# Optimization experiments

Measured on AMD Instinct MI355X. Metric: run time of the kernel, lower is better.

The kernel has to match this reference:

```python
import jax, jax.numpy as jnp
import numpy as np

D_MODEL = 1024
SEQ_LEN = 2048
NUM_EIGH = 24
BATCH = 4


def _spectral_filters(L, K):
    # Hankel matrix Z[i,j] = 2 / ((i+j)^3 - (i+j)), 1-indexed; top-K eigvecs scaled by sigma^0.25
    t = np.arange(1, L + 1, dtype=np.float64)
    s = t[:, None] + t[None, :]
    Z = 2.0 / (s ** 3 - s)
    sigma, phi = np.linalg.eigh(Z)
    phi_k = phi[:, -K:] * (sigma[-K:] ** 0.25)
    return jnp.asarray(phi_k, dtype=jnp.float32)


def setup_inputs() -> dict:
    key = jax.random.key(0)
    k1, k2, k3 = jax.random.split(key, 3)
    std = 1.0 / np.sqrt(D_MODEL)
    return {
        "x": jax.random.normal(k1, (BATCH, SEQ_LEN, D_MODEL), dtype=jnp.float32),
        "M_inputs": jax.random.normal(k2, (D_MODEL, D_MODEL), dtype=jnp.float32) * std,
        "M_filters": jax.random.normal(k3, (NUM_EIGH, D_MODEL), dtype=jnp.float32) * std,
        "phi": _spectral_filters(SEQ_LEN, NUM_EIGH),
    }


def _convolve_approx(u, v, n):
    # u: [B, L, D] inputs (already projected); v: [L, D] per-channel causal filters.
    # Dual-branch causal FFT convolution:
    #   plus[b,t,d]  = sum_{s<=t} v[s,d] * u[b,t-s,d]
    #   minus[b,t,d] = (-1)^t * sum_{s<=t} v[s,d] * (-1)^{t-s} u[b,t-s,d]
    B, L, D = u.shape
    sgn = jnp.where(jnp.arange(L) % 2 == 0, 1.0, -1.0).astype(u.dtype)[None, :, None]  # [1,L,1]
    V = jnp.fft.rfft(v, n=n, axis=0)                     # [F, D] complex
    U = jnp.stack([u, u * sgn], axis=-1)                 # [B, L, D, 2]
    Uf = jnp.fft.rfft(U, n=n, axis=1)                    # [B, F, D, 2]
    conv = jnp.fft.irfft(V[None, :, :, None] * Uf, n=n, axis=1)[:, :L]  # [B, L, D, 2]
    return conv[..., 0], conv[..., 1] * sgn


def reference(x, M_inputs, M_filters, phi):
    L = x.shape[1]
    n = 1 << int(np.ceil(np.log2(2 * L - 1)))  # next pow2 of 2L-1 (static)
    x_proj = x @ M_inputs                       # [B, L, D]
    phi_proj = phi[:L] @ M_filters              # [L, D]
    spectral_plus, spectral_minus = _convolve_approx(x_proj, phi_proj, n)
    return spectral_plus + spectral_minus
```

## Files before the change

kernel.cpp:

```cpp
#include <hip/hip_runtime.h>
#include <stdint.h>

#define D_MODEL 1024
#define SEQ 2048
#define HALF 1024
#define K_EIG 24
#define GUARD4 24
#define K4 128
#define K4P (GUARD4 + K4)
#define WE_JP4 72

typedef __attribute__((ext_vector_type(8))) short bf16x8;
typedef __attribute__((ext_vector_type(4))) float f32x4;
typedef _Float16 f16;
typedef _Float16 f16x2 __attribute__((ext_vector_type(2)));
typedef unsigned int uint;

#define GAS __attribute__((address_space(1)))
#define LAS __attribute__((address_space(3)))

static __device__ __forceinline__ unsigned short f2bf(float f) {
  union { float f; uint32_t u; } v; v.f = f;
  uint32_t u = v.u;
  u += 0x7FFFu + ((u >> 16) & 1u);
  return (unsigned short)(u >> 16);
}

static __device__ __forceinline__ float dot2(uint w2, uint u2, float c) {
  return __builtin_amdgcn_fdot2(__builtin_bit_cast(f16x2, w2),
                                __builtin_bit_cast(f16x2, u2), c, false);
}

static __device__ __forceinline__ uint pkrtz(float lo, float hi) {
  return __builtin_bit_cast(uint, __builtin_amdgcn_cvt_pkrtz(lo, hi));
}

static __device__ __forceinline__ uint pkbf(float lo, float hi) {
  return (uint)f2bf(lo) | ((uint)f2bf(hi) << 16);
}

__global__ void k_zero_guard(uint4* __restrict__ u4) {
  int idx = blockIdx.x * 256 + threadIdx.x;
  int r = blockIdx.y;
  u4[(size_t)r * (K4P * 1024) + idx] = make_uint4(0u, 0u, 0u, 0u);
}

__global__ void k_transpose_M(const float* __restrict__ M, unsigned short* __restrict__ Mt) {
  __shared__ float tile[32][33];
  int k0 = blockIdx.y * 32, n0 = blockIdx.x * 32;
  int tx = threadIdx.x & 31, ty = threadIdx.x >> 5;
  #pragma unroll
  for (int r = 0; r < 32; r += 8)
    tile[ty + r][tx] = M[(size_t)(k0 + ty + r) * D_MODEL + n0 + tx];
  __syncthreads();
  #pragma unroll
  for (int r = 0; r < 32; r += 8)
    Mt[(size_t)(n0 + ty + r) * D_MODEL + k0 + tx] = f2bf(tile[tx][ty + r]);
}

__global__ __launch_bounds__(256) void k_we4(const float* __restrict__ phi,
                                             const float* __restrict__ Mf,
                                             uint4* __restrict__ we4) {
  const int jp4 = blockIdx.x;
  const int d = blockIdx.y * 256 + threadIdx.x;
  if (jp4 >= 64) {
    we4[(size_t)jp4 * D_MODEL + d] = make_uint4(0u, 0u, 0u, 0u);
    return;
  }
  __shared__ float ph[8][K_EIG];
  if (threadIdx.x < 8 * K_EIG) {
    int s = threadIdx.x / K_EIG, k = threadIdx.x - s * K_EIG;
    ph[s][k] = phi[(size_t)(16 * jp4 + 2 * s) * K_EIG + k];
  }
  __syncthreads();
  float s[8] = {};
  #pragma unroll
  for (int k = 0; k < K_EIG; ++k) {
    float mv = Mf[(size_t)k * D_MODEL + d];
    #pragma unroll
    for (int j = 0; j < 8; ++j) s[j] = fmaf(ph[j][k], mv, s[j]);
  }
  uint4 o;
  o.x = pkrtz(2.f * s[0], 2.f * s[1]);
  o.y = pkrtz(2.f * s[2], 2.f * s[3]);
  o.z = pkrtz(2.f * s[4], 2.f * s[5]);
  o.w = pkrtz(2.f * s[6], 2.f * s[7]);
  we4[(size_t)jp4 * D_MODEL + d] = o;
}

__global__ __launch_bounds__(256) void k_gemm(const float* __restrict__ X,
                                              const unsigned short* __restrict__ Bt,
                                              uint* __restrict__ Ug) {
  __shared__ float Asf[128 * 32];
  __shared__ unsigned short Bs[128 * 32];
  const int bid = (int)blockIdx.x;
  const int swz = (bid & 7) * 64 + (bid >> 3);
  const int m0 = (swz >> 3) * 128;
  const int n0 = (swz & 7) * 128;
  const int tid = threadIdx.x;
  const int lane = tid & 63;
  const int wave = tid >> 6;
  const int wm = wave >> 1, wn = wave & 1;
  const int qo = lane >> 4;

  const int a_row = lane >> 3;
  const int a_chunk = (lane & 7) ^ a_row;
  const int b_row = lane >> 2;
  const int b_chunk = (lane & 3) ^ (b_row & 3);

  f32x4 acc[4][4] = {};

  for (int k0 = 0; k0 < 1024; k0 += 32) {
    __syncthreads();
    #pragma unroll
    for (int c = 0; c < 4; ++c) {
      int rbase = wave * 32 + c * 8;
      const float* src = X + (size_t)(m0 + rbase + a_row) * 1024 + k0 + a_chunk * 4;
      __builtin_amdgcn_global_load_lds((const GAS void*)src, (LAS void*)(Asf + rbase * 32), 16, 0, 0);
    }
    #pragma unroll
    for (int c = 0; c < 2; ++c) {
      int rbase = wave * 32 + c * 16;
      const unsigned short* src = Bt + (size_t)(n0 + rbase + b_row) * 1024 + k0 + b_chunk * 8;
      __builtin_amdgcn_global_load_lds((const GAS void*)src, (LAS void*)(Bs + rbase * 32), 16, 0, 0);
    }
    __syncthreads();

    bf16x8 a[4], b[4];
    #pragma unroll
    for (int mt = 0; mt < 4; ++mt) {
      int m = wm * 64 + mt * 16 + (lane & 15);
      const float* base = Asf + m * 32;
      int s0 = (2 * qo) ^ (lane & 7);
      int s1 = s0 ^ 1;
      float4 f0 = *(const float4*)(base + s0 * 4);
      float4 f1 = *(const float4*)(base + s1 * 4);
      uint4 pk;
      pk.x = pkbf(f0.x, f0.y); pk.y = pkbf(f0.z, f0.w);
      pk.z = pkbf(f1.x, f1.y); pk.w = pkbf(f1.z, f1.w);
      a[mt] = __builtin_bit_cast(bf16x8, pk);
    }
    #pragma unroll
    for (int nt = 0; nt < 4; ++nt) {
      int n = wn * 64 + nt * 16 + (lane & 15);
      int sb = qo ^ (lane & 3);
      b[nt] = *(const bf16x8*)(Bs + n * 32 + sb * 8);
    }
    #pragma unroll
    for (int mt = 0; mt < 4; ++mt)
      #pragma unroll
      for (int nt = 0; nt < 4; ++nt)
        acc[mt][nt] = __builtin_amdgcn_mfma_f32_16x16x32_bf16(a[mt], b[nt], acc[mt][nt], 0, 0, 0);
  }

  const int crow = (lane >> 4) * 4;
  const int ccol = lane & 15;
  #pragma unroll
  for (int mt = 0; mt < 4; ++mt) {
    int m = m0 + wm * 64 + mt * 16 + crow;
    int b_ = m >> 11;
    int t0 = m & 2047;
    int r_e = b_ << 1;
    int k4 = t0 >> 4;
    int dwo = (t0 >> 2) & 3;
    size_t base_e = ((size_t)(r_e * K4P + GUARD4 + k4) * 1024) * 4 + dwo;
    size_t base_o = ((size_t)((r_e + 1) * K4P + GUARD4 + k4) * 1024) * 4 + dwo;
    #pragma unroll
    for (int nt = 0; nt < 4; ++nt) {
      int n = n0 + wn * 64 + nt * 16 + ccol;
      Ug[base_e + (size_t)n * 4] = pkrtz(acc[mt][nt][0], acc[mt][nt][2]);
      Ug[base_o + (size_t)n * 4] = pkrtz(acc[mt][nt][1], acc[mt][nt][3]);
    }
  }
}

__global__ __launch_bounds__(512, 6) void k_conv(const uint4* __restrict__ u4,
                                                 const uint4* __restrict__ we4,
                                                 float* __restrict__ out) {
  __shared__ uint4 u_r[32 * 64];
  __shared__ uint4 w_s[2][8][64];
  const int flat = blockIdx.x;
  const int dt = flat & 15;
  const int r  = (flat >> 4) & 7;
  const int a  = 7 - (flat >> 7);
  const int d0 = dt * 64;
  const int tid = threadIdx.x;
  const int dl = tid & 63;
  const int ig = tid >> 6;

  const uint4* ub = u4 + ((size_t)r * K4P + GUARD4) * 1024 + d0;
  const int b_ = r >> 1, p = r & 1;

#define STAGEU(k40)                                                                     \
  {                                                                                     \
    int k4e = (k40) + ig;                                                               \
    const uint4* src = ub + (long long)k4e * 1024 + dl;                                 \
    __builtin_amdgcn_global_load_lds((const GAS void*)src,                              \
                                     (LAS void*)(u_r + (k4e & 31) * 64), 16, 0, 0);     \
  }

#define STAGEW(ch)                                                                      \
  {                                                                                     \
    const uint4* src = we4 + (size_t)((ch) * 8 + ig) * 1024 + d0 + dl;                  \
    __builtin_amdgcn_global_load_lds((const GAS void*)src,                              \
                                     (LAS void*)(&w_s[(ch) & 1][ig][0]), 16, 0, 0);     \
  }

  const int i0 = a * 128;
  const int ibase = i0 + ig * 16;
  const int niter = (2 * a + 2) < 8 ? (2 * a + 2) : 8;

  STAGEU(16 * a - 8); STAGEU(16 * a); STAGEU(16 * a + 8);
  STAGEW(0);
  __syncthreads();

  float acc[16];
#pragma unroll
  for (int o = 0; o < 16; ++o) acc[o] = 0.f;

#pragma unroll 1
  for (int c = 0; c < niter; ++c) {
    STAGEU(16 * a - 8 * c - 16);
    STAGEW(c + 1);
    const int cb = c & 1;
    const int kbase = 16 * a + 2 * ig - 8 * c - 2;
#pragma unroll
    for (int s = 0; s < 4; ++s) {
      const int kb = kbase - 2 * s;
      uint4 v0 = u_r[((kb + 0) & 31) * 64 + dl];
      uint4 v1 = u_r[((kb + 1) & 31) * 64 + dl];
      uint4 v2 = u_r[((kb + 2) & 31) * 64 + dl];
      uint4 v3 = u_r[((kb + 3) & 31) * 64 + dl];
      uint P[16];
      P[0] = v0.x; P[1] = v0.y; P[2] = v0.z; P[3] = v0.w;
      P[4] = v1.x; P[5] = v1.y; P[6] = v1.z; P[7] = v1.w;
      P[8] = v2.x; P[9] = v2.y; P[10] = v2.z; P[11] = v2.w;
      P[12] = v3.x; P[13] = v3.y; P[14] = v3.z; P[15] = v3.w;
      uint4 wv0 = w_s[cb][2 * s][dl];
      uint4 wv1 = w_s[cb][2 * s + 1][dl];
      uint W[8];
      W[0] = wv0.x; W[1] = wv0.y; W[2] = wv0.z; W[3] = wv0.w;
      W[4] = wv1.x; W[5] = wv1.y; W[6] = wv1.z; W[7] = wv1.w;
      uint WS[8];
#pragma unroll
      for (int q = 0; q < 8; ++q) WS[q] = __builtin_amdgcn_alignbit(W[q], W[q], 16);
      uint pe[15];
#pragma unroll
      for (int j = 0; j < 15; ++j) pe[j] = __builtin_amdgcn_perm(P[j + 1], P[j], 0x03020504u);
#pragma unroll
      for (int q = 0; q < 8; ++q) {
#pragma unroll
        for (int h = 0; h < 8; ++h) {
          acc[2 * h]     = dot2(W[q],  pe[7 - q + h], acc[2 * h]);
          acc[2 * h + 1] = dot2(WS[q], P[8 - q + h],  acc[2 * h + 1]);
        }
      }
    }
    __syncthreads();
  }

#pragma unroll
  for (int o = 0; o < 16; ++o)
    out[((size_t)b_ * SEQ + 2 * (ibase + o) + p) * D_MODEL + d0 + dl] = acc[o];
#undef STAGEU
#undef STAGEW
}

extern "C" void kernel_launch(void* const* d_in, const int* in_sizes, int n_in,
                              void* d_out, int out_size, void* d_ws, size_t ws_size,
                              hipStream_t stream) {
  const float* x   = (const float*)d_in[0];
  const float* Mi  = (const float*)d_in[1];
  const float* Mf  = (const float*)d_in[2];
  const float* phi = (const float*)d_in[3];
  float* out = (float*)d_out;

  unsigned short* Mt = (unsigned short*)d_out;

  char* ws = (char*)d_ws;
  uint4* we4 = (uint4*)(ws);
  uint4* u4  = (uint4*)(ws + (2u << 20));

  hipLaunchKernelGGL(k_zero_guard, dim3(96, 8), dim3(256), 0, stream, u4);
  hipLaunchKernelGGL(k_transpose_M, dim3(32, 32), dim3(256), 0, stream, Mi, Mt);
  hipLaunchKernelGGL(k_we4, dim3(72, 4), dim3(256), 0, stream, phi, Mf, we4);
  hipLaunchKernelGGL(k_gemm, dim3(512), dim3(256), 0, stream, x, Mt, (uint*)u4);
  hipLaunchKernelGGL(k_conv, dim3(1024), dim3(512), 0, stream, u4, we4, out);
}
```

Before: 124.0 us.

## Merge prep kernels into one launch and double-buffer GEMM LDS staging

```diff
diff --git a/kernel.cpp b/kernel.cpp
--- a/kernel.cpp
+++ b/kernel.cpp
@@ -39,60 +39,71 @@
   return (uint)f2bf(lo) | ((uint)f2bf(hi) << 16);
 }
 
-__global__ void k_zero_guard(uint4* __restrict__ u4) {
-  int idx = blockIdx.x * 256 + threadIdx.x;
-  int r = blockIdx.y;
-  u4[(size_t)r * (K4P * 1024) + idx] = make_uint4(0u, 0u, 0u, 0u);
-}
-
-__global__ void k_transpose_M(const float* __restrict__ M, unsigned short* __restrict__ Mt) {
-  __shared__ float tile[32][33];
-  int k0 = blockIdx.y * 32, n0 = blockIdx.x * 32;
-  int tx = threadIdx.x & 31, ty = threadIdx.x >> 5;
-  #pragma unroll
-  for (int r = 0; r < 32; r += 8)
-    tile[ty + r][tx] = M[(size_t)(k0 + ty + r) * D_MODEL + n0 + tx];
-  __syncthreads();
-  #pragma unroll
-  for (int r = 0; r < 32; r += 8)
-    Mt[(size_t)(n0 + ty + r) * D_MODEL + k0 + tx] = f2bf(tile[tx][ty + r]);
-}
-
-__global__ __launch_bounds__(256) void k_we4(const float* __restrict__ phi,
-                                             const float* __restrict__ Mf,
-                                             uint4* __restrict__ we4) {
-  const int jp4 = blockIdx.x;
-  const int d = blockIdx.y * 256 + threadIdx.x;
-  if (jp4 >= 64) {
-    we4[(size_t)jp4 * D_MODEL + d] = make_uint4(0u, 0u, 0u, 0u);
+__global__ __launch_bounds__(256) void k_prep(const float* __restrict__ Mi,
+                                              const float* __restrict__ phi,
+                                              const float* __restrict__ Mf,
+                                              uint4* __restrict__ u4,
+                                              unsigned short* __restrict__ Mt,
+                                              uint4* __restrict__ we4) {
+  __shared__ float smem[1056];
+  const int blk = (int)blockIdx.x;
+  const int tidx = threadIdx.x;
+
+  if (blk < 768) {
+    int r = blk / 96;
+    int idx = (blk - r * 96) * 256 + tidx;
+    u4[(size_t)r * (K4P * 1024) + idx] = make_uint4(0u, 0u, 0u, 0u);
     return;
   }
-  __shared__ float ph[8][K_EIG];
-  if (threadIdx.x < 8 * K_EIG) {
-    int s = threadIdx.x / K_EIG, k = threadIdx.x - s * K_EIG;
-    ph[s][k] = phi[(size_t)(16 * jp4 + 2 * s) * K_EIG + k];
-  }
-  __syncthreads();
-  float s[8] = {};
-  #pragma unroll
-  for (int k = 0; k < K_EIG; ++k) {
-    float mv = Mf[(size_t)k * D_MODEL + d];
-    #pragma unroll
-    for (int j = 0; j < 8; ++j) s[j] = fmaf(ph[j][k], mv, s[j]);
-  }
-  uint4 o;
-  o.x = pkrtz(2.f * s[0], 2.f * s[1]);
-  o.y = pkrtz(2.f * s[2], 2.f * s[3]);
-  o.z = pkrtz(2.f * s[4], 2.f * s[5]);
-  o.w = pkrtz(2.f * s[6], 2.f * s[7]);
-  we4[(size_t)jp4 * D_MODEL + d] = o;
+  if (blk < 1792) {
+    int bidx = blk - 768;
+    int n0 = (bidx & 31) * 32, k0 = (bidx >> 5) * 32;
+    float (*tile)[33] = (float(*)[33])smem;
+    int tx = tidx & 31, ty = tidx >> 5;
+    #pragma unroll
+    for (int r = 0; r < 32; r += 8)
+      tile[ty + r][tx] = Mi[(size_t)(k0 + ty + r) * D_MODEL + n0 + tx];
+    __syncthreads();
+    #pragma unroll
+    for (int r = 0; r < 32; r += 8)
+      Mt[(size_t)(n0 + ty + r) * D_MODEL + k0 + tx] = f2bf(tile[tx][ty + r]);
+    return;
+  }
+  {
+    int bidx = blk - 1792;
+    int jp4 = bidx % 72;
+    int d = (bidx / 72) * 256 + tidx;
+    if (jp4 >= 64) {
+      we4[(size_t)jp4 * D_MODEL + d] = make_uint4(0u, 0u, 0u, 0u);
+      return;
+    }
+    float (*ph)[K_EIG] = (float(*)[K_EIG])smem;
+    if (tidx < 8 * K_EIG) {
+      int s = tidx / K_EIG, k = tidx - s * K_EIG;
+      ph[s][k] = phi[(size_t)(16 * jp4 + 2 * s) * K_EIG + k];
+    }
+    __syncthreads();
+    float s[8] = {};
+    #pragma unroll
+    for (int k = 0; k < K_EIG; ++k) {
+      float mv = Mf[(size_t)k * D_MODEL + d];
+      #pragma unroll
+      for (int j = 0; j < 8; ++j) s[j] = fmaf(ph[j][k], mv, s[j]);
+    }
+    uint4 o;
+    o.x = pkrtz(2.f * s[0], 2.f * s[1]);
+    o.y = pkrtz(2.f * s[2], 2.f * s[3]);
+    o.z = pkrtz(2.f * s[4], 2.f * s[5]);
+    o.w = pkrtz(2.f * s[6], 2.f * s[7]);
+    we4[(size_t)jp4 * D_MODEL + d] = o;
+  }
 }
 
 __global__ __launch_bounds__(256) void k_gemm(const float* __restrict__ X,
                                               const unsigned short* __restrict__ Bt,
                                               uint* __restrict__ Ug) {
-  __shared__ float Asf[128 * 32];
-  __shared__ unsigned short Bs[128 * 32];
+  __shared__ float Asf[2][128 * 32];
+  __shared__ unsigned short Bs[2][128 * 32];
   const int bid = (int)blockIdx.x;
   const int swz = (bid & 7) * 64 + (bid >> 3);
   const int m0 = (swz >> 3) * 128;
@@ -108,29 +119,37 @@
   const int b_row = lane >> 2;
   const int b_chunk = (lane & 3) ^ (b_row & 3);
 
+#define GSTAGE(buf, k0v)                                                                  \
+  {                                                                                       \
+    _Pragma("unroll") for (int c = 0; c < 4; ++c) {                                       \
+      int rbase = wave * 32 + c * 8;                                                      \
+      const float* srcA = X + (size_t)(m0 + rbase + a_row) * 1024 + (k0v) + a_chunk * 4;  \
+      __builtin_amdgcn_global_load_lds((const GAS void*)srcA,                             \
+                                       (LAS void*)(Asf[buf] + rbase * 32), 16, 0, 0);     \
+    }                                                                                     \
+    _Pragma("unroll") for (int c = 0; c < 2; ++c) {                                       \
+      int rbase = wave * 32 + c * 16;                                                     \
+      const unsigned short* srcB = Bt + (size_t)(n0 + rbase + b_row) * 1024 + (k0v) + b_chunk * 8; \
+      __builtin_amdgcn_global_load_lds((const GAS void*)srcB,                             \
+                                       (LAS void*)(Bs[buf] + rbase * 32), 16, 0, 0);      \
+    }                                                                                     \
+  }
+
   f32x4 acc[4][4] = {};
 
-  for (int k0 = 0; k0 < 1024; k0 += 32) {
-    __syncthreads();
-    #pragma unroll
-    for (int c = 0; c < 4; ++c) {
-      int rbase = wave * 32 + c * 8;
-      const float* src = X + (size_t)(m0 + rbase + a_row) * 1024 + k0 + a_chunk * 4;
-      __builtin_amdgcn_global_load_lds((const GAS void*)src, (LAS void*)(Asf + rbase * 32), 16, 0, 0);
-    }
-    #pragma unroll
-    for (int c = 0; c < 2; ++c) {
-      int rbase = wave * 32 + c * 16;
-      const unsigned short* src = Bt + (size_t)(n0 + rbase + b_row) * 1024 + k0 + b_chunk * 8;
-      __builtin_amdgcn_global_load_lds((const GAS void*)src, (LAS void*)(Bs + rbase * 32), 16, 0, 0);
-    }
-    __syncthreads();
+  GSTAGE(0, 0);
+  __syncthreads();
+
+#pragma unroll 1
+  for (int t = 0; t < 32; ++t) {
+    const int cur = t & 1;
+    if (t < 31) GSTAGE(cur ^ 1, (t + 1) * 32);
 
     bf16x8 a[4], b[4];
     #pragma unroll
     for (int mt = 0; mt < 4; ++mt) {
       int m = wm * 64 + mt * 16 + (lane & 15);
-      const float* base = Asf + m * 32;
+      const float* base = Asf[cur] + m * 32;
       int s0 = (2 * qo) ^ (lane & 7);
       int s1 = s0 ^ 1;
       float4 f0 = *(const float4*)(base + s0 * 4);
@@ -144,14 +163,17 @@
     for (int nt = 0; nt < 4; ++nt) {
       int n = wn * 64 + nt * 16 + (lane & 15);
       int sb = qo ^ (lane & 3);
-      b[nt] = *(const bf16x8*)(Bs + n * 32 + sb * 8);
+      b[nt] = *(const bf16x8*)(Bs[cur] + n * 32 + sb * 8);
     }
     #pragma unroll
     for (int mt = 0; mt < 4; ++mt)
       #pragma unroll
       for (int nt = 0; nt < 4; ++nt)
         acc[mt][nt] = __builtin_amdgcn_mfma_f32_16x16x32_bf16(a[mt], b[nt], acc[mt][nt], 0, 0, 0);
-  }
+
+    __syncthreads();
+  }
+#undef GSTAGE
 
   const int crow = (lane >> 4) * 4;
   const int ccol = lane & 15;
@@ -281,9 +303,7 @@
   uint4* we4 = (uint4*)(ws);
   uint4* u4  = (uint4*)(ws + (2u << 20));
 
-  hipLaunchKernelGGL(k_zero_guard, dim3(96, 8), dim3(256), 0, stream, u4);
-  hipLaunchKernelGGL(k_transpose_M, dim3(32, 32), dim3(256), 0, stream, Mi, Mt);
-  hipLaunchKernelGGL(k_we4, dim3(72, 4), dim3(256), 0, stream, phi, Mf, we4);
+  hipLaunchKernelGGL(k_prep, dim3(2080), dim3(256), 0, stream, Mi, phi, Mf, u4, Mt, we4);
   hipLaunchKernelGGL(k_gemm, dim3(512), dim3(256), 0, stream, x, Mt, (uint*)u4);
   hipLaunchKernelGGL(k_conv, dim3(1024), dim3(512), 0, stream, u4, we4, out);
 }
```

Result: faster. 117.6 us (-5.2%).
